# Kernel tuning notes

Measured on AMD Instinct MI355X. Metric: run time of the kernel, lower is better.

The kernel has to match this reference:

```python
import jax, jax.numpy as jnp
import numpy as np

B, T, I, H = 64, 512, 512, 1024
NUM_LAYERS_LIQ = 1
DT = 0.1


def setup_inputs() -> dict:
    key = jax.random.key(0)
    ks = jax.random.split(key, 10)
    s = 1.0 / np.sqrt(H)
    f32 = jnp.float32
    return {
        "x": jax.random.normal(ks[0], (B, T, I), f32),
        # LSTM params (PyTorch layout: gates ordered i, f, g, o)
        "W_ih": jax.random.uniform(ks[1], (4 * H, I), f32, -s, s),
        "W_hh": jax.random.uniform(ks[2], (4 * H, H), f32, -s, s),
        "b_ih": jax.random.uniform(ks[3], (4 * H,), f32, -s, s),
        "b_hh": jax.random.uniform(ks[4], (4 * H,), f32, -s, s),
        # liquid cell params
        "W_in": jax.random.uniform(ks[5], (H, H), f32, -s, s),
        "b_in": jax.random.uniform(ks[6], (H,), f32, -s, s),
        "W_rec": jax.random.uniform(ks[7], (H, H), f32, -s, s),
        "b_rec": jax.random.uniform(ks[8], (H,), f32, -s, s),
        "tau": jnp.ones((H,), f32) * 0.5,
    }


def _forward(x, W_ih, W_hh, b_ih, b_hh, W_in, b_in, W_rec, b_rec, tau):
    Bb, Tt, _ = x.shape
    Hh = W_hh.shape[1]
    # Precompute input contribution to all gates: [T, B, 4H] (time-major for scan)
    gx = jnp.einsum('bti,gi->tbg', x, W_ih) + b_ih + b_hh

    def lstm_step(carry, gx_t):
        h, c = carry
        g = gx_t + h @ W_hh.T
        i, f, gg, o = jnp.split(g, 4, axis=-1)
        c = jax.nn.sigmoid(f) * c + jax.nn.sigmoid(i) * jnp.tanh(gg)
        h = jax.nn.sigmoid(o) * jnp.tanh(c)
        return (h, c), h

    h0 = jnp.zeros((Bb, Hh), x.dtype)
    _, ys = jax.lax.scan(lstm_step, (h0, h0), gx)  # ys: [T, B, H]

    # Liquid-time-constant layer over LSTM outputs
    tau_c = jnp.clip(tau, 0.1, 5.0)
    leak = DT / tau_c  # [H]
    xi = jnp.einsum('tbh,gh->tbg', ys, W_in) + b_in  # fc_in applied to every step

    def liq_step(h, xi_t):
        for _ in range(NUM_LAYERS_LIQ):
            act = jnp.tanh(xi_t + h @ W_rec.T + b_rec)
            h = h + leak * (act - h)
        return h, None

    h_final, _ = jax.lax.scan(liq_step, h0, xi)
    return h_final  # [B, H]


def reference(x, W_ih, W_hh, b_ih, b_hh, W_in, b_in, W_rec, b_rec, tau):
    return _forward(x, W_ih, W_hh, b_ih, b_hh, W_in, b_in, W_rec, b_rec, tau)
```

## Files before the change

### kernel.cpp

```cpp
#include <hip/hip_runtime.h>
#include <hip/hip_bf16.h>
#include <math.h>

#define B_ 64
#define T_ 512
#define I_ 512
#define H_ 1024

__global__ __launch_bounds__(256) void gemm_bt_bias(
    const float* __restrict__ A, const float* __restrict__ Bt,
    const float* __restrict__ bias1, const float* __restrict__ bias2,
    float* __restrict__ C, int N, int K, long s1, long s2)
{
  __shared__ float As[8][132];
  __shared__ float Bs[8][132];
  const int t   = threadIdx.x;
  const int r0  = blockIdx.y * 128;
  const int n0  = blockIdx.x * 128;
  const int lm  = t >> 1;
  const int lk4 = (t & 1) * 4;
  const int tm0 = (t >> 4) * 8;
  const int tn0 = (t & 15) * 8;

  float acc[8][8] = {};

  for (int k0 = 0; k0 < K; k0 += 8) {
    const int r = r0 + lm;
    const float4 a = *(const float4*)(A + (long)(r & 63) * s1 + (long)(r >> 6) * s2 + k0 + lk4);
    const float4 b = *(const float4*)(Bt + (long)(n0 + lm) * K + k0 + lk4);
    As[lk4 + 0][lm] = a.x; As[lk4 + 1][lm] = a.y; As[lk4 + 2][lm] = a.z; As[lk4 + 3][lm] = a.w;
    Bs[lk4 + 0][lm] = b.x; Bs[lk4 + 1][lm] = b.y; Bs[lk4 + 2][lm] = b.z; Bs[lk4 + 3][lm] = b.w;
    __syncthreads();
#pragma unroll
    for (int kk = 0; kk < 8; ++kk) {
      const float4 a0 = *(const float4*)&As[kk][tm0];
      const float4 a1 = *(const float4*)&As[kk][tm0 + 4];
      const float4 b0 = *(const float4*)&Bs[kk][tn0];
      const float4 b1 = *(const float4*)&Bs[kk][tn0 + 4];
      const float am[8] = {a0.x, a0.y, a0.z, a0.w, a1.x, a1.y, a1.z, a1.w};
      const float bn[8] = {b0.x, b0.y, b0.z, b0.w, b1.x, b1.y, b1.z, b1.w};
#pragma unroll
      for (int i = 0; i < 8; ++i)
#pragma unroll
        for (int j = 0; j < 8; ++j)
          acc[i][j] = fmaf(am[i], bn[j], acc[i][j]);
    }
    __syncthreads();
  }

  float bs[8];
#pragma unroll
  for (int j = 0; j < 8; ++j) {
    const int n = n0 + tn0 + j;
    bs[j] = bias1[n] + (bias2 ? bias2[n] : 0.f);
  }
#pragma unroll
  for (int i = 0; i < 8; ++i) {
    const long r = r0 + tm0 + i;
    const float4 v0 = make_float4(acc[i][0] + bs[0], acc[i][1] + bs[1],
                                  acc[i][2] + bs[2], acc[i][3] + bs[3]);
    const float4 v1 = make_float4(acc[i][4] + bs[4], acc[i][5] + bs[5],
                                  acc[i][6] + bs[6], acc[i][7] + bs[7]);
    *(float4*)(C + r * N + n0 + tn0)     = v0;
    *(float4*)(C + r * N + n0 + tn0 + 4) = v1;
  }
}

__device__ __forceinline__ void grid_barrier(unsigned* cnt, unsigned target)
{
  __syncthreads();
  if (threadIdx.x == 0) {
    __threadfence();
    __hip_atomic_fetch_add(cnt, 1u, __ATOMIC_ACQ_REL, __HIP_MEMORY_SCOPE_AGENT);
    while (__hip_atomic_load(cnt, __ATOMIC_ACQUIRE, __HIP_MEMORY_SCOPE_AGENT) < target)
      __builtin_amdgcn_s_sleep(1);
    __threadfence();
  }
  __syncthreads();
}

__device__ __forceinline__ float sel4(float a, float b, float c, float d, int u)
{
  return (u & 2) ? ((u & 1) ? d : c) : ((u & 1) ? b : a);
}

__global__ __launch_bounds__(256) void lstm_scan(
    const float* __restrict__ W_hh, const float* __restrict__ gx,
    float* __restrict__ ys, float* __restrict__ hA, float* __restrict__ hB,
    float* __restrict__ cbuf, unsigned* __restrict__ cnt, int base, int nsteps)
{
  __shared__ float Wl[16][1040];
  const int wg = blockIdx.x, t = threadIdx.x;
  {
    const int ru = t >> 4, l16 = t & 15;
    const int q = ru >> 2, uu = ru & 3;
    const float* src = W_hh + (long)(q * H_ + wg * 4 + uu) * H_;
#pragma unroll
    for (int j = 0; j < 16; ++j) {
      const int k = l16 * 4 + j * 64;
      *(float4*)&Wl[ru][(k >> 8) * 260 + (k & 255)] = *(const float4*)(src + k);
    }
  }
  __syncthreads();

  const int b = t >> 2, u = t & 3;
  const int unit = wg * 4 + u;
  float creg = cbuf[b * H_ + unit];

  for (int ls = 0; ls < nsteps; ++ls) {
    const float* hp = (ls & 1) ? hB : hA;
    float*       hn = (ls & 1) ? hA : hB;
    const float* hq = hp + b * H_ + u * 256;
    const float* wq = &Wl[0][0] + u * 260;

    float p[4][4] = {};
#pragma unroll 2
    for (int k4 = 0; k4 < 64; ++k4) {
      const float4 hv = *(const float4*)(hq + k4 * 4);
#pragma unroll
      for (int r = 0; r < 16; ++r) {
        const float4 wv = *(const float4*)(wq + r * 1040 + k4 * 4);
        float& a = p[r >> 2][r & 3];
        a = fmaf(hv.x, wv.x, a); a = fmaf(hv.y, wv.y, a);
        a = fmaf(hv.z, wv.z, a); a = fmaf(hv.w, wv.w, a);
      }
    }
#pragma unroll
    for (int q = 0; q < 4; ++q)
#pragma unroll
      for (int uu = 0; uu < 4; ++uu) {
        p[q][uu] += __shfl_xor(p[q][uu], 1, 64);
        p[q][uu] += __shfl_xor(p[q][uu], 2, 64);
      }
    const float* gp = gx + (long)ls * (B_ * 4 * H_) + b * (4 * H_);
    const float gi = sel4(p[0][0], p[0][1], p[0][2], p[0][3], u) + gp[unit];
    const float gf = sel4(p[1][0], p[1][1], p[1][2], p[1][3], u) + gp[H_ + unit];
    const float gg = sel4(p[2][0], p[2][1], p[2][2], p[2][3], u) + gp[2 * H_ + unit];
    const float go = sel4(p[3][0], p[3][1], p[3][2], p[3][3], u) + gp[3 * H_ + unit];
    const float si = 1.f / (1.f + __expf(-gi));
    const float sf = 1.f / (1.f + __expf(-gf));
    const float so = 1.f / (1.f + __expf(-go));
    const float tg = tanhf(gg);
    creg = sf * creg + si * tg;
    const float hv_ = so * tanhf(creg);
    hn[b * H_ + unit] = hv_;
    ys[(long)ls * (B_ * H_) + b * H_ + unit] = hv_;
    grid_barrier(cnt, (unsigned)(base + ls + 1) * 256u);
  }
  cbuf[b * H_ + unit] = creg;
}

__global__ __launch_bounds__(256) void liq_scan(
    const float* __restrict__ W_rec, const float* __restrict__ xi,
    const float* __restrict__ b_rec, const float* __restrict__ tau,
    float* __restrict__ hA, float* __restrict__ hB, float* __restrict__ out,
    unsigned* __restrict__ cnt, int base, int nsteps)
{
  __shared__ float Wl[4][1040];
  const int wg = blockIdx.x, t = threadIdx.x;
  {
    const int ru = t >> 6, c0 = (t & 63) * 4;
    const float* src = W_rec + (long)(wg * 4 + ru) * H_;
#pragma unroll
    for (int j = 0; j < 4; ++j)
      *(float4*)&Wl[ru][j * 260 + c0] = *(const float4*)(src + c0 + j * 256);
  }
  __syncthreads();

  const int b = t >> 2, u = t & 3;
  const int unit = wg * 4 + u;
  const float tc   = fminf(fmaxf(tau[unit], 0.1f), 5.0f);
  const float leak = 0.1f / tc;
  const float br   = b_rec[unit];
  float hlast = 0.f;

  for (int ls = 0; ls < nsteps; ++ls) {
    const float* hp = (ls & 1) ? hB : hA;
    float*       hn = (ls & 1) ? hA : hB;
    const float* hrow = hp + b * H_;
    const float* hq = hrow + u * 256;
    const float* wq = &Wl[0][0] + u * 260;
    float p0 = 0.f, p1 = 0.f, p2 = 0.f, p3 = 0.f;
#pragma unroll 4
    for (int k4 = 0; k4 < 64; ++k4) {
      const float4 hv = *(const float4*)(hq + k4 * 4);
      const float4 w0 = *(const float4*)(wq + 0 * 1040 + k4 * 4);
      const float4 w1 = *(const float4*)(wq + 1 * 1040 + k4 * 4);
      const float4 w2 = *(const float4*)(wq + 2 * 1040 + k4 * 4);
      const float4 w3 = *(const float4*)(wq + 3 * 1040 + k4 * 4);
      p0 = fmaf(hv.x, w0.x, p0); p0 = fmaf(hv.y, w0.y, p0);
      p0 = fmaf(hv.z, w0.z, p0); p0 = fmaf(hv.w, w0.w, p0);
      p1 = fmaf(hv.x, w1.x, p1); p1 = fmaf(hv.y, w1.y, p1);
      p1 = fmaf(hv.z, w1.z, p1); p1 = fmaf(hv.w, w1.w, p1);
      p2 = fmaf(hv.x, w2.x, p2); p2 = fmaf(hv.y, w2.y, p2);
      p2 = fmaf(hv.z, w2.z, p2); p2 = fmaf(hv.w, w2.w, p2);
      p3 = fmaf(hv.x, w3.x, p3); p3 = fmaf(hv.y, w3.y, p3);
      p3 = fmaf(hv.w, w3.w, p3); p3 = fmaf(hv.z, w3.z, p3);
    }
    p0 += __shfl_xor(p0, 1, 64); p0 += __shfl_xor(p0, 2, 64);
    p1 += __shfl_xor(p1, 1, 64); p1 += __shfl_xor(p1, 2, 64);
    p2 += __shfl_xor(p2, 1, 64); p2 += __shfl_xor(p2, 2, 64);
    p3 += __shfl_xor(p3, 1, 64); p3 += __shfl_xor(p3, 2, 64);
    const float acc = sel4(p0, p1, p2, p3, u);
    const float hself = hrow[unit];
    const float act = tanhf(xi[(long)ls * (B_ * H_) + b * H_ + unit] + acc + br);
    const float hnew = hself + leak * (act - hself);
    hn[b * H_ + unit] = hnew;
    hlast = hnew;
    grid_barrier(cnt, (unsigned)(base + ls + 1) * 256u);
  }
  out[b * H_ + unit] = hlast;
}

extern "C" void kernel_launch(void* const* d_in, const int* in_sizes, int n_in,
                              void* d_out, int out_size, void* d_ws, size_t ws_size,
                              hipStream_t stream)
{
  (void)in_sizes; (void)n_in; (void)out_size;
  const float* x     = (const float*)d_in[0];
  const float* W_ih  = (const float*)d_in[1];
  const float* W_hh  = (const float*)d_in[2];
  const float* b_ih  = (const float*)d_in[3];
  const float* b_hh  = (const float*)d_in[4];
  const float* W_in  = (const float*)d_in[5];
  const float* b_in  = (const float*)d_in[6];
  const float* W_rec = (const float*)d_in[7];
  const float* b_rec = (const float*)d_in[8];
  const float* tau   = (const float*)d_in[9];

  const size_t HB   = (size_t)B_ * H_ * sizeof(float);
  const size_t TAIL = 5 * HB + 1024;

  int Tc = T_;
  while (Tc > 2) {
    const size_t need = (size_t)Tc * B_ * 4 * H_ * 4
                      + (size_t)Tc * B_ * H_ * 4
                      + TAIL;
    if (need <= ws_size) break;
    Tc >>= 1;
  }

  char* ws = (char*)d_ws;
  const size_t GXB = (size_t)Tc * B_ * 4 * H_ * sizeof(float);
  const size_t YSB = (size_t)Tc * B_ * H_ * sizeof(float);
  float* gx   = (float*)ws;
  float* ys   = (float*)(ws + GXB);
  char*  tail = ws + GXB + YSB;
  float* cbuf = (float*)(tail);
  float* hA   = (float*)(tail + 1 * HB);
  float* hB   = (float*)(tail + 2 * HB);
  float* hLA  = (float*)(tail + 3 * HB);
  float* hLB  = (float*)(tail + 4 * HB);
  unsigned* cntS = (unsigned*)(tail + 5 * HB);
  unsigned* cntL = (unsigned*)(tail + 5 * HB + 256);
  float* outp = (float*)d_out;

  hipMemsetAsync(tail, 0, TAIL, stream);

  const int nch = T_ / Tc;
  for (int k = 0; k < nch; ++k) {
    int t0 = k * Tc;
    int ns = Tc;

    gemm_bt_bias<<<dim3(4 * H_ / 128, Tc * B_ / 128), 256, 0, stream>>>(
        x + (long)t0 * I_, W_ih, b_ih, b_hh, gx, 4 * H_, I_,
        (long)T_ * I_, (long)I_);

    {
      void* args[] = {(void*)&W_hh, (void*)&gx, (void*)&ys, (void*)&hA,
                      (void*)&hB, (void*)&cbuf, (void*)&cntS, (void*)&t0, (void*)&ns};
      hipLaunchCooperativeKernel((void*)lstm_scan, dim3(256), dim3(256),
                                 args, 0, stream);
    }

    gemm_bt_bias<<<dim3(H_ / 128, Tc * B_ / 128), 256, 0, stream>>>(
        ys, W_in, b_in, nullptr, gx, H_, H_, (long)H_, (long)(B_ * H_));

    {
      void* args[] = {(void*)&W_rec, (void*)&gx, (void*)&b_rec, (void*)&tau,
                      (void*)&hLA, (void*)&hLB, (void*)&outp, (void*)&cntL,
                      (void*)&t0, (void*)&ns};
      hipLaunchCooperativeKernel((void*)liq_scan, dim3(256), dim3(256),
                                 args, 0, stream);
    }
  }
}
```

Measured before the change: 39.59 ms.

## Fuse LSTM and liquid scans into one cooperative kernel with flag barrier

Merges the LSTM recurrence, the W_in projection and the liquid recurrence into a single persistent cooperative kernel. The liquid step for timestep s-1 is computed alongside LSTM step s, which removes one of the two serial grid-synchronised scans, the ys buffer and the second GEMM. The atomic-counter grid barrier is replaced by a per-workgroup flag array gathered by a master workgroup that then writes a release word. In exchange each step does more FMA work and LDS reads, the LDS footprint grows, and the barrier's latency now depends on one master workgroup.

```diff
diff --git a/kernel.cpp b/kernel.cpp
--- a/kernel.cpp
+++ b/kernel.cpp
@@ -66,17 +66,32 @@
   }
 }
 
-__device__ __forceinline__ void grid_barrier(unsigned* cnt, unsigned target)
-{
+__device__ __forceinline__ void grid_barrier(unsigned* flags, unsigned* rel,
+                                             int wg, unsigned target)
+{
+  __threadfence();
   __syncthreads();
-  if (threadIdx.x == 0) {
-    __threadfence();
-    __hip_atomic_fetch_add(cnt, 1u, __ATOMIC_ACQ_REL, __HIP_MEMORY_SCOPE_AGENT);
-    while (__hip_atomic_load(cnt, __ATOMIC_ACQUIRE, __HIP_MEMORY_SCOPE_AGENT) < target)
-      __builtin_amdgcn_s_sleep(1);
-    __threadfence();
-  }
-  __syncthreads();
+  const int tid = threadIdx.x;
+  if (wg == 0) {
+    if (tid >= 1) {
+      while (__hip_atomic_load(flags + tid * 32, __ATOMIC_ACQUIRE,
+                               __HIP_MEMORY_SCOPE_AGENT) < target)
+        __builtin_amdgcn_s_sleep(1);
+    }
+    __syncthreads();
+    if (tid == 0)
+      __hip_atomic_store(rel, target, __ATOMIC_RELEASE, __HIP_MEMORY_SCOPE_AGENT);
+  } else {
+    if (tid == 0) {
+      __hip_atomic_store(flags + wg * 32, target, __ATOMIC_RELEASE,
+                         __HIP_MEMORY_SCOPE_AGENT);
+      while (__hip_atomic_load(rel, __ATOMIC_ACQUIRE,
+                               __HIP_MEMORY_SCOPE_AGENT) < target)
+        __builtin_amdgcn_s_sleep(1);
+    }
+    __syncthreads();
+  }
+  __threadfence();
 }
 
 __device__ __forceinline__ float sel4(float a, float b, float c, float d, int u)
@@ -84,12 +99,20 @@
   return (u & 2) ? ((u & 1) ? d : c) : ((u & 1) ? b : a);
 }
 
-__global__ __launch_bounds__(256) void lstm_scan(
-    const float* __restrict__ W_hh, const float* __restrict__ gx,
-    float* __restrict__ ys, float* __restrict__ hA, float* __restrict__ hB,
-    float* __restrict__ cbuf, unsigned* __restrict__ cnt, int base, int nsteps)
-{
-  __shared__ float Wl[16][1040];
+__global__ __launch_bounds__(256) void fused_scan(
+    const float* __restrict__ W_hh, const float* __restrict__ W_in,
+    const float* __restrict__ W_rec, const float* __restrict__ gx,
+    const float* __restrict__ b_in, const float* __restrict__ b_rec,
+    const float* __restrict__ tau,
+    float* __restrict__ hA, float* __restrict__ hB,
+    float* __restrict__ hLA, float* __restrict__ hLB,
+    float* __restrict__ cbuf, float* __restrict__ out,
+    unsigned* __restrict__ flags, unsigned* __restrict__ rel,
+    int base, int nsteps, int do_epi)
+{
+  __shared__ float Whh[16][1040];
+  __shared__ float Win[4][1040];
+  __shared__ float Wrc[4][1040];
   const int wg = blockIdx.x, t = threadIdx.x;
   {
     const int ru = t >> 4, l16 = t & 15;
@@ -98,7 +121,18 @@
 #pragma unroll
     for (int j = 0; j < 16; ++j) {
       const int k = l16 * 4 + j * 64;
-      *(float4*)&Wl[ru][(k >> 8) * 260 + (k & 255)] = *(const float4*)(src + k);
+      *(float4*)&Whh[ru][(k >> 8) * 260 + (k & 255)] = *(const float4*)(src + k);
+    }
+  }
+  {
+    const int ru = t >> 6, c0 = (t & 63) * 4;
+    const float* si = W_in  + (long)(wg * 4 + ru) * H_;
+    const float* sr = W_rec + (long)(wg * 4 + ru) * H_;
+#pragma unroll
+    for (int j = 0; j < 4; ++j) {
+      Win[ru][j * 260 + c0 + 0] = 0.f;
+      *(float4*)&Win[ru][j * 260 + c0] = *(const float4*)(si + c0 + j * 256);
+      *(float4*)&Wrc[ru][j * 260 + c0] = *(const float4*)(sr + c0 + j * 256);
     }
   }
   __syncthreads();
@@ -106,17 +140,32 @@
   const int b = t >> 2, u = t & 3;
   const int unit = wg * 4 + u;
   float creg = cbuf[b * H_ + unit];
+  const float tc   = fminf(fmaxf(tau[unit], 0.1f), 5.0f);
+  const float leak = 0.1f / tc;
+  const float br   = b_rec[unit];
+  const float bi   = b_in[unit];
+
+  const float* wq  = &Whh[0][0] + u * 260;
+  const float* wiq = &Win[0][0] + u * 260;
+  const float* wrq = &Wrc[0][0] + u * 260;
 
   for (int ls = 0; ls < nsteps; ++ls) {
-    const float* hp = (ls & 1) ? hB : hA;
-    float*       hn = (ls & 1) ? hA : hB;
-    const float* hq = hp + b * H_ + u * 256;
-    const float* wq = &Wl[0][0] + u * 260;
+    const int s = base + ls;
+    const int j = s - 1;
+    const float* hp  = (s & 1) ? hB : hA;
+    float*       hn  = (s & 1) ? hA : hB;
+    const float* hLp = (j & 1) ? hLB : hLA;
+    float*       hLn = (j & 1) ? hLA : hLB;
+    const float* hq  = hp  + b * H_ + u * 256;
+    const float* hLq = hLp + b * H_ + u * 256;
 
     float p[4][4] = {};
+    float qi[4] = {};
+    float rr[4] = {};
 #pragma unroll 2
     for (int k4 = 0; k4 < 64; ++k4) {
-      const float4 hv = *(const float4*)(hq + k4 * 4);
+      const float4 hv  = *(const float4*)(hq  + k4 * 4);
+      const float4 hlv = *(const float4*)(hLq + k4 * 4);
 #pragma unroll
       for (int r = 0; r < 16; ++r) {
         const float4 wv = *(const float4*)(wq + r * 1040 + k4 * 4);
@@ -124,14 +173,34 @@
         a = fmaf(hv.x, wv.x, a); a = fmaf(hv.y, wv.y, a);
         a = fmaf(hv.z, wv.z, a); a = fmaf(hv.w, wv.w, a);
       }
-    }
-#pragma unroll
-    for (int q = 0; q < 4; ++q)
+#pragma unroll
+      for (int r = 0; r < 4; ++r) {
+        const float4 wv = *(const float4*)(wiq + r * 1040 + k4 * 4);
+        float& a = qi[r];
+        a = fmaf(hv.x, wv.x, a); a = fmaf(hv.y, wv.y, a);
+        a = fmaf(hv.z, wv.z, a); a = fmaf(hv.w, wv.w, a);
+      }
+#pragma unroll
+      for (int r = 0; r < 4; ++r) {
+        const float4 wv = *(const float4*)(wrq + r * 1040 + k4 * 4);
+        float& a = rr[r];
+        a = fmaf(hlv.x, wv.x, a); a = fmaf(hlv.y, wv.y, a);
+        a = fmaf(hlv.z, wv.z, a); a = fmaf(hlv.w, wv.w, a);
+      }
+    }
+#pragma unroll
+    for (int g = 0; g < 4; ++g)
 #pragma unroll
       for (int uu = 0; uu < 4; ++uu) {
-        p[q][uu] += __shfl_xor(p[q][uu], 1, 64);
-        p[q][uu] += __shfl_xor(p[q][uu], 2, 64);
-      }
+        p[g][uu] += __shfl_xor(p[g][uu], 1, 64);
+        p[g][uu] += __shfl_xor(p[g][uu], 2, 64);
+      }
+#pragma unroll
+    for (int r = 0; r < 4; ++r) {
+      qi[r] += __shfl_xor(qi[r], 1, 64); qi[r] += __shfl_xor(qi[r], 2, 64);
+      rr[r] += __shfl_xor(rr[r], 1, 64); rr[r] += __shfl_xor(rr[r], 2, 64);
+    }
+
     const float* gp = gx + (long)ls * (B_ * 4 * H_) + b * (4 * H_);
     const float gi = sel4(p[0][0], p[0][1], p[0][2], p[0][3], u) + gp[unit];
     const float gf = sel4(p[1][0], p[1][1], p[1][2], p[1][3], u) + gp[H_ + unit];
@@ -142,74 +211,54 @@
     const float so = 1.f / (1.f + __expf(-go));
     const float tg = tanhf(gg);
     creg = sf * creg + si * tg;
-    const float hv_ = so * tanhf(creg);
-    hn[b * H_ + unit] = hv_;
-    ys[(long)ls * (B_ * H_) + b * H_ + unit] = hv_;
-    grid_barrier(cnt, (unsigned)(base + ls + 1) * 256u);
+    hn[b * H_ + unit] = so * tanhf(creg);
+
+    if (s > 0) {
+      const float xi    = sel4(qi[0], qi[1], qi[2], qi[3], u) + bi;
+      const float rec   = sel4(rr[0], rr[1], rr[2], rr[3], u);
+      const float hself = hLp[b * H_ + unit];
+      const float act   = tanhf(xi + rec + br);
+      hLn[b * H_ + unit] = hself + leak * (act - hself);
+    }
+
+    grid_barrier(flags, rel, wg, (unsigned)(s + 1));
   }
   cbuf[b * H_ + unit] = creg;
-}
-
-__global__ __launch_bounds__(256) void liq_scan(
-    const float* __restrict__ W_rec, const float* __restrict__ xi,
-    const float* __restrict__ b_rec, const float* __restrict__ tau,
-    float* __restrict__ hA, float* __restrict__ hB, float* __restrict__ out,
-    unsigned* __restrict__ cnt, int base, int nsteps)
-{
-  __shared__ float Wl[4][1040];
-  const int wg = blockIdx.x, t = threadIdx.x;
-  {
-    const int ru = t >> 6, c0 = (t & 63) * 4;
-    const float* src = W_rec + (long)(wg * 4 + ru) * H_;
-#pragma unroll
-    for (int j = 0; j < 4; ++j)
-      *(float4*)&Wl[ru][j * 260 + c0] = *(const float4*)(src + c0 + j * 256);
-  }
-  __syncthreads();
-
-  const int b = t >> 2, u = t & 3;
-  const int unit = wg * 4 + u;
-  const float tc   = fminf(fmaxf(tau[unit], 0.1f), 5.0f);
-  const float leak = 0.1f / tc;
-  const float br   = b_rec[unit];
-  float hlast = 0.f;
-
-  for (int ls = 0; ls < nsteps; ++ls) {
-    const float* hp = (ls & 1) ? hB : hA;
-    float*       hn = (ls & 1) ? hA : hB;
-    const float* hrow = hp + b * H_;
-    const float* hq = hrow + u * 256;
-    const float* wq = &Wl[0][0] + u * 260;
-    float p0 = 0.f, p1 = 0.f, p2 = 0.f, p3 = 0.f;
+
+  if (do_epi) {
+    const int j = base + nsteps - 1;
+    const float* hp  = (j & 1) ? hA : hB;
+    const float* hLp = (j & 1) ? hLB : hLA;
+    const float* hq  = hp  + b * H_ + u * 256;
+    const float* hLq = hLp + b * H_ + u * 256;
+    float qi[4] = {}, rr[4] = {};
 #pragma unroll 4
     for (int k4 = 0; k4 < 64; ++k4) {
-      const float4 hv = *(const float4*)(hq + k4 * 4);
-      const float4 w0 = *(const float4*)(wq + 0 * 1040 + k4 * 4);
-      const float4 w1 = *(const float4*)(wq + 1 * 1040 + k4 * 4);
-      const float4 w2 = *(const float4*)(wq + 2 * 1040 + k4 * 4);
-      const float4 w3 = *(const float4*)(wq + 3 * 1040 + k4 * 4);
-      p0 = fmaf(hv.x, w0.x, p0); p0 = fmaf(hv.y, w0.y, p0);
-      p0 = fmaf(hv.z, w0.z, p0); p0 = fmaf(hv.w, w0.w, p0);
-      p1 = fmaf(hv.x, w1.x, p1); p1 = fmaf(hv.y, w1.y, p1);
-      p1 = fmaf(hv.z, w1.z, p1); p1 = fmaf(hv.w, w1.w, p1);
-      p2 = fmaf(hv.x, w2.x, p2); p2 = fmaf(hv.y, w2.y, p2);
-      p2 = fmaf(hv.z, w2.z, p2); p2 = fmaf(hv.w, w2.w, p2);
-      p3 = fmaf(hv.x, w3.x, p3); p3 = fmaf(hv.y, w3.y, p3);
-      p3 = fmaf(hv.w, w3.w, p3); p3 = fmaf(hv.z, w3.z, p3);
-    }
-    p0 += __shfl_xor(p0, 1, 64); p0 += __shfl_xor(p0, 2, 64);
-    p1 += __shfl_xor(p1, 1, 64); p1 += __shfl_xor(p1, 2, 64);
-    p2 += __shfl_xor(p2, 1, 64); p2 += __shfl_xor(p2, 2, 64);
-    p3 += __shfl_xor(p3, 1, 64); p3 += __shfl_xor(p3, 2, 64);
-    const float acc = sel4(p0, p1, p2, p3, u);
-    const float hself = hrow[unit];
-    const float act = tanhf(xi[(long)ls * (B_ * H_) + b * H_ + unit] + acc + br);
-    const float hnew = hself + leak * (act - hself);
-    hn[b * H_ + unit] = hnew;
-    hlast = hnew;
-    grid_barrier(cnt, (unsigned)(base + ls + 1) * 256u);
-  }
-  out[b * H_ + unit] = hlast;
+      const float4 hv  = *(const float4*)(hq  + k4 * 4);
+      const float4 hlv = *(const float4*)(hLq + k4 * 4);
+#pragma unroll
+      for (int r = 0; r < 4; ++r) {
+        const float4 wv = *(const float4*)(wiq + r * 1040 + k4 * 4);
+        const float4 wr = *(const float4*)(wrq + r * 1040 + k4 * 4);
+        float& a = qi[r];
+        a = fmaf(hv.x, wv.x, a); a = fmaf(hv.y, wv.y, a);
+        a = fmaf(hv.z, wv.z, a); a = fmaf(hv.w, wv.w, a);
+        float& c = rr[r];
+        c = fmaf(hlv.x, wr.x, c); c = fmaf(hlv.y, wr.y, c);
+        c = fmaf(hlv.z, wr.z, c); c = fmaf(hlv.w, wr.w, c);
+      }
+    }
+#pragma unroll
+    for (int r = 0; r < 4; ++r) {
+      qi[r] += __shfl_xor(qi[r], 1, 64); qi[r] += __shfl_xor(qi[r], 2, 64);
+      rr[r] += __shfl_xor(rr[r], 1, 64); rr[r] += __shfl_xor(rr[r], 2, 64);
+    }
+    const float xi    = sel4(qi[0], qi[1], qi[2], qi[3], u) + bi;
+    const float rec   = sel4(rr[0], rr[1], rr[2], rr[3], u);
+    const float hself = hLp[b * H_ + unit];
+    const float act   = tanhf(xi + rec + br);
+    out[b * H_ + unit] = hself + leak * (act - hself);
+  }
 }
 
 extern "C" void kernel_launch(void* const* d_in, const int* in_sizes, int n_in,
@@ -229,30 +278,27 @@
   const float* tau   = (const float*)d_in[9];
 
   const size_t HB   = (size_t)B_ * H_ * sizeof(float);
-  const size_t TAIL = 5 * HB + 1024;
+  const size_t FLB  = 256 * 128 + 256;
+  const size_t TAIL = 5 * HB + FLB;
 
   int Tc = T_;
   while (Tc > 2) {
-    const size_t need = (size_t)Tc * B_ * 4 * H_ * 4
-                      + (size_t)Tc * B_ * H_ * 4
-                      + TAIL;
+    const size_t need = (size_t)Tc * B_ * 4 * H_ * 4 + TAIL;
     if (need <= ws_size) break;
     Tc >>= 1;
   }
 
   char* ws = (char*)d_ws;
   const size_t GXB = (size_t)Tc * B_ * 4 * H_ * sizeof(float);
-  const size_t YSB = (size_t)Tc * B_ * H_ * sizeof(float);
   float* gx   = (float*)ws;
-  float* ys   = (float*)(ws + GXB);
-  char*  tail = ws + GXB + YSB;
+  char*  tail = ws + GXB;
   float* cbuf = (float*)(tail);
   float* hA   = (float*)(tail + 1 * HB);
   float* hB   = (float*)(tail + 2 * HB);
   float* hLA  = (float*)(tail + 3 * HB);
   float* hLB  = (float*)(tail + 4 * HB);
-  unsigned* cntS = (unsigned*)(tail + 5 * HB);
-  unsigned* cntL = (unsigned*)(tail + 5 * HB + 256);
+  unsigned* flags = (unsigned*)(tail + 5 * HB);
+  unsigned* rel   = (unsigned*)(tail + 5 * HB + 256 * 128);
   float* outp = (float*)d_out;
 
   hipMemsetAsync(tail, 0, TAIL, stream);
@@ -261,27 +307,20 @@
   for (int k = 0; k < nch; ++k) {
     int t0 = k * Tc;
     int ns = Tc;
+    int epi = (k == nch - 1) ? 1 : 0;
 
     gemm_bt_bias<<<dim3(4 * H_ / 128, Tc * B_ / 128), 256, 0, stream>>>(
         x + (long)t0 * I_, W_ih, b_ih, b_hh, gx, 4 * H_, I_,
         (long)T_ * I_, (long)I_);
 
     {
-      void* args[] = {(void*)&W_hh, (void*)&gx, (void*)&ys, (void*)&hA,
-                      (void*)&hB, (void*)&cbuf, (void*)&cntS, (void*)&t0, (void*)&ns};
-      hipLaunchCooperativeKernel((void*)lstm_scan, dim3(256), dim3(256),
+      void* args[] = {(void*)&W_hh, (void*)&W_in, (void*)&W_rec, (void*)&gx,
+                      (void*)&b_in, (void*)&b_rec, (void*)&tau,
+                      (void*)&hA, (void*)&hB, (void*)&hLA, (void*)&hLB,
+                      (void*)&cbuf, (void*)&outp, (void*)&flags, (void*)&rel,
+                      (void*)&t0, (void*)&ns, (void*)&epi};
+      hipLaunchCooperativeKernel((void*)fused_scan, dim3(256), dim3(256),
                                  args, 0, stream);
     }
-
-    gemm_bt_bias<<<dim3(H_ / 128, Tc * B_ / 128), 256, 0, stream>>>(
-        ys, W_in, b_in, nullptr, gx, H_, H_, (long)H_, (long)(B_ * H_));
-
-    {
-      void* args[] = {(void*)&W_rec, (void*)&gx, (void*)&b_rec, (void*)&tau,
-                      (void*)&hLA, (void*)&hLB, (void*)&outp, (void*)&cntL,
-                      (void*)&t0, (void*)&ns};
-      hipLaunchCooperativeKernel((void*)liq_scan, dim3(256), dim3(256),
-                                 args, 0, stream);
-    }
-  }
-}
+  }
+}
```

After: 64.62 ms. +63.2%, slower.

## Fuse LSTM and liquid scans into one skewed cooperative kernel

Applied to the files above, without the earlier changes.

Merges the LSTM recurrence, the W_in projection and the liquid recurrence into a single persistent cooperative kernel. The liquid step runs one timestep behind the LSTM, so the W_in dot product on h_{t-1} is computed inside the same k-loop as W_hh, and an epilogue handles the final liquid step. This removes the ys buffer, the second GEMM and one full sequence of grid barriers. Each thread now handles 4 batch rows times 4 units for register reuse of the weights, at the cost of more LDS (24 rows) and more registers per thread, which could reduce occupancy or cause spills.

```diff
diff --git a/kernel.cpp b/kernel.cpp
--- a/kernel.cpp
+++ b/kernel.cpp
@@ -84,132 +84,198 @@
   return (u & 2) ? ((u & 1) ? d : c) : ((u & 1) ? b : a);
 }
 
-__global__ __launch_bounds__(256) void lstm_scan(
-    const float* __restrict__ W_hh, const float* __restrict__ gx,
-    float* __restrict__ ys, float* __restrict__ hA, float* __restrict__ hB,
-    float* __restrict__ cbuf, unsigned* __restrict__ cnt, int base, int nsteps)
-{
-  __shared__ float Wl[16][1040];
+__global__ __launch_bounds__(256) void fused_scan(
+    const float* __restrict__ W_hh, const float* __restrict__ W_in,
+    const float* __restrict__ W_rec, const float* __restrict__ gx,
+    const float* __restrict__ b_in, const float* __restrict__ b_rec,
+    const float* __restrict__ tau,
+    float* __restrict__ hA, float* __restrict__ hB,
+    float* __restrict__ hLA, float* __restrict__ hLB,
+    float* __restrict__ cbuf, float* __restrict__ out,
+    unsigned* __restrict__ cnt, int base, int nsteps, int do_epi)
+{
+  __shared__ float Wl[24][1044];
   const int wg = blockIdx.x, t = threadIdx.x;
+  const int u0 = wg * 4;
+
   {
-    const int ru = t >> 4, l16 = t & 15;
-    const int q = ru >> 2, uu = ru & 3;
-    const float* src = W_hh + (long)(q * H_ + wg * 4 + uu) * H_;
-#pragma unroll
-    for (int j = 0; j < 16; ++j) {
-      const int k = l16 * 4 + j * 64;
-      *(float4*)&Wl[ru][(k >> 8) * 260 + (k & 255)] = *(const float4*)(src + k);
+    const int k = t * 4;
+    const int dst = (k >> 8) * 260 + (k & 255);
+#pragma unroll
+    for (int j = 0; j < 24; ++j) {
+      const float* src;
+      if (j < 16)      src = W_hh  + ((long)(j & 3) * H_ + u0 + (j >> 2)) * H_;
+      else if (j < 20) src = W_in  + (long)(u0 + (j - 16)) * H_;
+      else             src = W_rec + (long)(u0 + (j - 20)) * H_;
+      *(float4*)&Wl[j][dst] = *(const float4*)(src + k);
     }
   }
   __syncthreads();
 
-  const int b = t >> 2, u = t & 3;
-  const int unit = wg * 4 + u;
-  float creg = cbuf[b * H_ + unit];
-
-  for (int ls = 0; ls < nsteps; ++ls) {
-    const float* hp = (ls & 1) ? hB : hA;
-    float*       hn = (ls & 1) ? hA : hB;
-    const float* hq = hp + b * H_ + u * 256;
-    const float* wq = &Wl[0][0] + u * 260;
-
-    float p[4][4] = {};
-#pragma unroll 2
-    for (int k4 = 0; k4 < 64; ++k4) {
-      const float4 hv = *(const float4*)(hq + k4 * 4);
-#pragma unroll
-      for (int r = 0; r < 16; ++r) {
-        const float4 wv = *(const float4*)(wq + r * 1040 + k4 * 4);
-        float& a = p[r >> 2][r & 3];
-        a = fmaf(hv.x, wv.x, a); a = fmaf(hv.y, wv.y, a);
-        a = fmaf(hv.z, wv.z, a); a = fmaf(hv.w, wv.w, a);
-      }
-    }
-#pragma unroll
-    for (int q = 0; q < 4; ++q)
-#pragma unroll
-      for (int uu = 0; uu < 4; ++uu) {
-        p[q][uu] += __shfl_xor(p[q][uu], 1, 64);
-        p[q][uu] += __shfl_xor(p[q][uu], 2, 64);
-      }
-    const float* gp = gx + (long)ls * (B_ * 4 * H_) + b * (4 * H_);
-    const float gi = sel4(p[0][0], p[0][1], p[0][2], p[0][3], u) + gp[unit];
-    const float gf = sel4(p[1][0], p[1][1], p[1][2], p[1][3], u) + gp[H_ + unit];
-    const float gg = sel4(p[2][0], p[2][1], p[2][2], p[2][3], u) + gp[2 * H_ + unit];
-    const float go = sel4(p[3][0], p[3][1], p[3][2], p[3][3], u) + gp[3 * H_ + unit];
-    const float si = 1.f / (1.f + __expf(-gi));
-    const float sf = 1.f / (1.f + __expf(-gf));
-    const float so = 1.f / (1.f + __expf(-go));
-    const float tg = tanhf(gg);
-    creg = sf * creg + si * tg;
-    const float hv_ = so * tanhf(creg);
-    hn[b * H_ + unit] = hv_;
-    ys[(long)ls * (B_ * H_) + b * H_ + unit] = hv_;
-    grid_barrier(cnt, (unsigned)(base + ls + 1) * 256u);
-  }
-  cbuf[b * H_ + unit] = creg;
-}
-
-__global__ __launch_bounds__(256) void liq_scan(
-    const float* __restrict__ W_rec, const float* __restrict__ xi,
-    const float* __restrict__ b_rec, const float* __restrict__ tau,
-    float* __restrict__ hA, float* __restrict__ hB, float* __restrict__ out,
-    unsigned* __restrict__ cnt, int base, int nsteps)
-{
-  __shared__ float Wl[4][1040];
-  const int wg = blockIdx.x, t = threadIdx.x;
-  {
-    const int ru = t >> 6, c0 = (t & 63) * 4;
-    const float* src = W_rec + (long)(wg * 4 + ru) * H_;
-#pragma unroll
-    for (int j = 0; j < 4; ++j)
-      *(float4*)&Wl[ru][j * 260 + c0] = *(const float4*)(src + c0 + j * 256);
-  }
-  __syncthreads();
-
-  const int b = t >> 2, u = t & 3;
-  const int unit = wg * 4 + u;
+  const int ug = t & 3;
+  const int u  = (t >> 2) & 3;
+  const int bg = t >> 4;
+  const int unit = u0 + ug;
+  const int b0 = bg * 4;
+
+  const float* wg0 = &Wl[ug * 4 + 0][u * 260];
+  const float* wg1 = &Wl[ug * 4 + 1][u * 260];
+  const float* wg2 = &Wl[ug * 4 + 2][u * 260];
+  const float* wg3 = &Wl[ug * 4 + 3][u * 260];
+  const float* wiq = &Wl[16 + ug][u * 260];
+  const float* wrq = &Wl[20 + ug][u * 260];
+
   const float tc   = fminf(fmaxf(tau[unit], 0.1f), 5.0f);
   const float leak = 0.1f / tc;
   const float br   = b_rec[unit];
-  float hlast = 0.f;
+  const float bi   = b_in[unit];
+
+  float c0 = cbuf[(long)(b0 + 0) * H_ + unit];
+  float c1 = cbuf[(long)(b0 + 1) * H_ + unit];
+  float c2 = cbuf[(long)(b0 + 2) * H_ + unit];
+  float c3 = cbuf[(long)(b0 + 3) * H_ + unit];
+  float s0 = hLB[(long)(b0 + 0) * H_ + unit];
+  float s1 = hLB[(long)(b0 + 1) * H_ + unit];
+  float s2 = hLB[(long)(b0 + 2) * H_ + unit];
+  float s3 = hLB[(long)(b0 + 3) * H_ + unit];
 
   for (int ls = 0; ls < nsteps; ++ls) {
-    const float* hp = (ls & 1) ? hB : hA;
-    float*       hn = (ls & 1) ? hA : hB;
-    const float* hrow = hp + b * H_;
-    const float* hq = hrow + u * 256;
-    const float* wq = &Wl[0][0] + u * 260;
-    float p0 = 0.f, p1 = 0.f, p2 = 0.f, p3 = 0.f;
+    const int s = base + ls;
+    const float* hp  = (s & 1) ? hB : hA;
+    float*       hn  = (s & 1) ? hA : hB;
+    const float* hLp = (s & 1) ? hLA : hLB;
+    float*       hLn = (s & 1) ? hLB : hLA;
+
+    const float* hq0 = hp  + (long)(b0 + 0) * H_ + u * 256;
+    const float* hq1 = hp  + (long)(b0 + 1) * H_ + u * 256;
+    const float* hq2 = hp  + (long)(b0 + 2) * H_ + u * 256;
+    const float* hq3 = hp  + (long)(b0 + 3) * H_ + u * 256;
+    const float* lq0 = hLp + (long)(b0 + 0) * H_ + u * 256;
+    const float* lq1 = hLp + (long)(b0 + 1) * H_ + u * 256;
+    const float* lq2 = hLp + (long)(b0 + 2) * H_ + u * 256;
+    const float* lq3 = hLp + (long)(b0 + 3) * H_ + u * 256;
+
+    float p00 = 0.f, p01 = 0.f, p02 = 0.f, p03 = 0.f;
+    float p10 = 0.f, p11 = 0.f, p12 = 0.f, p13 = 0.f;
+    float p20 = 0.f, p21 = 0.f, p22 = 0.f, p23 = 0.f;
+    float p30 = 0.f, p31 = 0.f, p32 = 0.f, p33 = 0.f;
+    float q0 = 0.f, q1 = 0.f, q2 = 0.f, q3 = 0.f;
+    float r0 = 0.f, r1 = 0.f, r2 = 0.f, r3 = 0.f;
+
+#define DOTBB(HQ, LQ, P0, P1, P2, P3, QQ, RR)                                  \
+    { const float4 hv = *(const float4*)(HQ + ko);                             \
+      const float4 lv = *(const float4*)(LQ + ko);                             \
+      P0 = fmaf(hv.x, a0.x, fmaf(hv.y, a0.y, fmaf(hv.z, a0.z, fmaf(hv.w, a0.w, P0)))); \
+      P1 = fmaf(hv.x, a1.x, fmaf(hv.y, a1.y, fmaf(hv.z, a1.z, fmaf(hv.w, a1.w, P1)))); \
+      P2 = fmaf(hv.x, a2.x, fmaf(hv.y, a2.y, fmaf(hv.z, a2.z, fmaf(hv.w, a2.w, P2)))); \
+      P3 = fmaf(hv.x, a3.x, fmaf(hv.y, a3.y, fmaf(hv.z, a3.z, fmaf(hv.w, a3.w, P3)))); \
+      QQ = fmaf(hv.x, wiv.x, fmaf(hv.y, wiv.y, fmaf(hv.z, wiv.z, fmaf(hv.w, wiv.w, QQ)))); \
+      RR = fmaf(lv.x, wrv.x, fmaf(lv.y, wrv.y, fmaf(lv.z, wrv.z, fmaf(lv.w, wrv.w, RR)))); }
+
+#pragma unroll 2
+    for (int k4 = 0; k4 < 64; ++k4) {
+      const int ko = k4 * 4;
+      const float4 a0  = *(const float4*)(wg0 + ko);
+      const float4 a1  = *(const float4*)(wg1 + ko);
+      const float4 a2  = *(const float4*)(wg2 + ko);
+      const float4 a3  = *(const float4*)(wg3 + ko);
+      const float4 wiv = *(const float4*)(wiq + ko);
+      const float4 wrv = *(const float4*)(wrq + ko);
+      DOTBB(hq0, lq0, p00, p10, p20, p30, q0, r0)
+      DOTBB(hq1, lq1, p01, p11, p21, p31, q1, r1)
+      DOTBB(hq2, lq2, p02, p12, p22, p32, q2, r2)
+      DOTBB(hq3, lq3, p03, p13, p23, p33, q3, r3)
+    }
+#undef DOTBB
+
+#define CMB(X) X += __shfl_xor(X, 4, 64); X += __shfl_xor(X, 8, 64);
+    CMB(p00) CMB(p01) CMB(p02) CMB(p03)
+    CMB(p10) CMB(p11) CMB(p12) CMB(p13)
+    CMB(p20) CMB(p21) CMB(p22) CMB(p23)
+    CMB(p30) CMB(p31) CMB(p32) CMB(p33)
+    CMB(q0) CMB(q1) CMB(q2) CMB(q3)
+    CMB(r0) CMB(r1) CMB(r2) CMB(r3)
+#undef CMB
+
+    float hn0, hn1, hn2, hn3;
+#define LSTM(bb, PI, PF, PG, PO, CC, HN)                                   \
+    { const float* gp = gx + ((long)ls * B_ + (b0 + bb)) * (4 * H_);       \
+      const float gi = PI + gp[unit];                                      \
+      const float gf = PF + gp[H_ + unit];                                 \
+      const float gg = PG + gp[2 * H_ + unit];                             \
+      const float go = PO + gp[3 * H_ + unit];                             \
+      const float si_ = 1.f / (1.f + __expf(-gi));                         \
+      const float sf_ = 1.f / (1.f + __expf(-gf));                         \
+      const float so_ = 1.f / (1.f + __expf(-go));                         \
+      CC = sf_ * CC + si_ * tanhf(gg);                                     \
+      HN = so_ * tanhf(CC); }
+    LSTM(0, p00, p10, p20, p30, c0, hn0)
+    LSTM(1, p01, p11, p21, p31, c1, hn1)
+    LSTM(2, p02, p12, p22, p32, c2, hn2)
+    LSTM(3, p03, p13, p23, p33, c3, hn3)
+#undef LSTM
+    hn[(long)(b0 + u) * H_ + unit] = sel4(hn0, hn1, hn2, hn3, u);
+
+    if (s > 0) {
+      const float a0_ = tanhf(q0 + bi + r0 + br);
+      const float a1_ = tanhf(q1 + bi + r1 + br);
+      const float a2_ = tanhf(q2 + bi + r2 + br);
+      const float a3_ = tanhf(q3 + bi + r3 + br);
+      s0 += leak * (a0_ - s0);
+      s1 += leak * (a1_ - s1);
+      s2 += leak * (a2_ - s2);
+      s3 += leak * (a3_ - s3);
+      hLn[(long)(b0 + u) * H_ + unit] = sel4(s0, s1, s2, s3, u);
+    }
+
+    grid_barrier(cnt, (unsigned)(s + 1) * 256u);
+  }
+  cbuf[(long)(b0 + u) * H_ + unit] = sel4(c0, c1, c2, c3, u);
+
+  if (do_epi) {
+    const int sl = base + nsteps - 1;
+    const float* hp  = (sl & 1) ? hA : hB;
+    const float* hLp = (sl & 1) ? hLB : hLA;
+    const float* hq0 = hp  + (long)(b0 + 0) * H_ + u * 256;
+    const float* hq1 = hp  + (long)(b0 + 1) * H_ + u * 256;
+    const float* hq2 = hp  + (long)(b0 + 2) * H_ + u * 256;
+    const float* hq3 = hp  + (long)(b0 + 3) * H_ + u * 256;
+    const float* lq0 = hLp + (long)(b0 + 0) * H_ + u * 256;
+    const float* lq1 = hLp + (long)(b0 + 1) * H_ + u * 256;
+    const float* lq2 = hLp + (long)(b0 + 2) * H_ + u * 256;
+    const float* lq3 = hLp + (long)(b0 + 3) * H_ + u * 256;
+    float q0 = 0.f, q1 = 0.f, q2 = 0.f, q3 = 0.f;
+    float r0 = 0.f, r1 = 0.f, r2 = 0.f, r3 = 0.f;
+#define EDOT(HQ, LQ, QQ, RR)                                                   \
+    { const float4 hv = *(const float4*)(HQ + ko);                             \
+      const float4 lv = *(const float4*)(LQ + ko);                             \
+      QQ = fmaf(hv.x, wiv.x, fmaf(hv.y, wiv.y, fmaf(hv.z, wiv.z, fmaf(hv.w, wiv.w, QQ)))); \
+      RR = fmaf(lv.x, wrv.x, fmaf(lv.y, wrv.y, fmaf(lv.z, wrv.z, fmaf(lv.w, wrv.w, RR)))); }
 #pragma unroll 4
     for (int k4 = 0; k4 < 64; ++k4) {
-      const float4 hv = *(const float4*)(hq + k4 * 4);
-      const float4 w0 = *(const float4*)(wq + 0 * 1040 + k4 * 4);
-      const float4 w1 = *(const float4*)(wq + 1 * 1040 + k4 * 4);
-      const float4 w2 = *(const float4*)(wq + 2 * 1040 + k4 * 4);
-      const float4 w3 = *(const float4*)(wq + 3 * 1040 + k4 * 4);
-      p0 = fmaf(hv.x, w0.x, p0); p0 = fmaf(hv.y, w0.y, p0);
-      p0 = fmaf(hv.z, w0.z, p0); p0 = fmaf(hv.w, w0.w, p0);
-      p1 = fmaf(hv.x, w1.x, p1); p1 = fmaf(hv.y, w1.y, p1);
-      p1 = fmaf(hv.z, w1.z, p1); p1 = fmaf(hv.w, w1.w, p1);
-      p2 = fmaf(hv.x, w2.x, p2); p2 = fmaf(hv.y, w2.y, p2);
-      p2 = fmaf(hv.z, w2.z, p2); p2 = fmaf(hv.w, w2.w, p2);
-      p3 = fmaf(hv.x, w3.x, p3); p3 = fmaf(hv.y, w3.y, p3);
-      p3 = fmaf(hv.w, w3.w, p3); p3 = fmaf(hv.z, w3.z, p3);
-    }
-    p0 += __shfl_xor(p0, 1, 64); p0 += __shfl_xor(p0, 2, 64);
-    p1 += __shfl_xor(p1, 1, 64); p1 += __shfl_xor(p1, 2, 64);
-    p2 += __shfl_xor(p2, 1, 64); p2 += __shfl_xor(p2, 2, 64);
-    p3 += __shfl_xor(p3, 1, 64); p3 += __shfl_xor(p3, 2, 64);
-    const float acc = sel4(p0, p1, p2, p3, u);
-    const float hself = hrow[unit];
-    const float act = tanhf(xi[(long)ls * (B_ * H_) + b * H_ + unit] + acc + br);
-    const float hnew = hself + leak * (act - hself);
-    hn[b * H_ + unit] = hnew;
-    hlast = hnew;
-    grid_barrier(cnt, (unsigned)(base + ls + 1) * 256u);
-  }
-  out[b * H_ + unit] = hlast;
+      const int ko = k4 * 4;
+      const float4 wiv = *(const float4*)(wiq + ko);
+      const float4 wrv = *(const float4*)(wrq + ko);
+      EDOT(hq0, lq0, q0, r0)
+      EDOT(hq1, lq1, q1, r1)
+      EDOT(hq2, lq2, q2, r2)
+      EDOT(hq3, lq3, q3, r3)
+    }
+#undef EDOT
+#define CMB(X) X += __shfl_xor(X, 4, 64); X += __shfl_xor(X, 8, 64);
+    CMB(q0) CMB(q1) CMB(q2) CMB(q3)
+    CMB(r0) CMB(r1) CMB(r2) CMB(r3)
+#undef CMB
+    const float a0_ = tanhf(q0 + bi + r0 + br);
+    const float a1_ = tanhf(q1 + bi + r1 + br);
+    const float a2_ = tanhf(q2 + bi + r2 + br);
+    const float a3_ = tanhf(q3 + bi + r3 + br);
+    const float o0 = s0 + leak * (a0_ - s0);
+    const float o1 = s1 + leak * (a1_ - s1);
+    const float o2 = s2 + leak * (a2_ - s2);
+    const float o3 = s3 + leak * (a3_ - s3);
+    out[(long)(b0 + u) * H_ + unit] = sel4(o0, o1, o2, o3, u);
+  }
 }
 
 extern "C" void kernel_launch(void* const* d_in, const int* in_sizes, int n_in,
@@ -233,26 +299,21 @@
 
   int Tc = T_;
   while (Tc > 2) {
-    const size_t need = (size_t)Tc * B_ * 4 * H_ * 4
-                      + (size_t)Tc * B_ * H_ * 4
-                      + TAIL;
+    const size_t need = (size_t)Tc * B_ * 4 * H_ * 4 + TAIL;
     if (need <= ws_size) break;
     Tc >>= 1;
   }
 
   char* ws = (char*)d_ws;
   const size_t GXB = (size_t)Tc * B_ * 4 * H_ * sizeof(float);
-  const size_t YSB = (size_t)Tc * B_ * H_ * sizeof(float);
   float* gx   = (float*)ws;
-  float* ys   = (float*)(ws + GXB);
-  char*  tail = ws + GXB + YSB;
+  char*  tail = ws + GXB;
   float* cbuf = (float*)(tail);
   float* hA   = (float*)(tail + 1 * HB);
   float* hB   = (float*)(tail + 2 * HB);
   float* hLA  = (float*)(tail + 3 * HB);
   float* hLB  = (float*)(tail + 4 * HB);
-  unsigned* cntS = (unsigned*)(tail + 5 * HB);
-  unsigned* cntL = (unsigned*)(tail + 5 * HB + 256);
+  unsigned* cnt = (unsigned*)(tail + 5 * HB);
   float* outp = (float*)d_out;
 
   hipMemsetAsync(tail, 0, TAIL, stream);
@@ -261,27 +322,20 @@
   for (int k = 0; k < nch; ++k) {
     int t0 = k * Tc;
     int ns = Tc;
+    int epi = (k == nch - 1) ? 1 : 0;
 
     gemm_bt_bias<<<dim3(4 * H_ / 128, Tc * B_ / 128), 256, 0, stream>>>(
         x + (long)t0 * I_, W_ih, b_ih, b_hh, gx, 4 * H_, I_,
         (long)T_ * I_, (long)I_);
 
     {
-      void* args[] = {(void*)&W_hh, (void*)&gx, (void*)&ys, (void*)&hA,
-                      (void*)&hB, (void*)&cbuf, (void*)&cntS, (void*)&t0, (void*)&ns};
-      hipLaunchCooperativeKernel((void*)lstm_scan, dim3(256), dim3(256),
+      void* args[] = {(void*)&W_hh, (void*)&W_in, (void*)&W_rec, (void*)&gx,
+                      (void*)&b_in, (void*)&b_rec, (void*)&tau,
+                      (void*)&hA, (void*)&hB, (void*)&hLA, (void*)&hLB,
+                      (void*)&cbuf, (void*)&outp, (void*)&cnt,
+                      (void*)&t0, (void*)&ns, (void*)&epi};
+      hipLaunchCooperativeKernel((void*)fused_scan, dim3(256), dim3(256),
                                  args, 0, stream);
     }
-
-    gemm_bt_bias<<<dim3(H_ / 128, Tc * B_ / 128), 256, 0, stream>>>(
-        ys, W_in, b_in, nullptr, gx, H_, H_, (long)H_, (long)(B_ * H_));
-
-    {
-      void* args[] = {(void*)&W_rec, (void*)&gx, (void*)&b_rec, (void*)&tau,
-                      (void*)&hLA, (void*)&hLB, (void*)&outp, (void*)&cntL,
-                      (void*)&t0, (void*)&ns};
-      hipLaunchCooperativeKernel((void*)liq_scan, dim3(256), dim3(256),
-                                 args, 0, stream);
-    }
-  }
-}
+  }
+}
```

After: 34.17 ms. 1.16x faster.
